# Performance work log

Measured on AMD Instinct MI355X. Metric: run time of the kernel, lower is better.

## Reference

```python
import jax, jax.numpy as jnp
import numpy as np

B, N, D_ATOM, HID, L = 32, 64, 5, 256, 9
E = N * N
F_E = 2 * HID + 2  # [h_i, h_j, d^2, edge_attr]


def _gather(x, idx):
    # x: (B, N, D), idx: (B, E) -> (B, E, D)
    return jax.vmap(lambda a, i: a[i])(x, idx)


def _segsum(data, idx, n):
    # per-batch unsorted segment sum over destination node idx
    return jax.vmap(lambda d, i: jax.ops.segment_sum(d, i, num_segments=n))(data, idx)


def _safe_dist(diff):
    # sqrt of squared norm, safe at 0 (masked self-edges) for grads
    return jnp.sqrt(jnp.maximum(jnp.sum(diff ** 2, axis=-1, keepdims=True), 1e-12))


def _remove_mean(x, mask):
    n = jnp.sum(mask, axis=1, keepdims=True)
    return (x - jnp.sum(x, axis=1, keepdims=True) / n) * mask


def setup_inputs() -> dict:
    key = jax.random.key(0)
    ks = iter(jax.random.split(key, 32))

    def W(shape):
        return jax.random.normal(next(ks), shape, jnp.float32) * 0.02

    x_in = jax.random.normal(next(ks), (B, N, 3), jnp.float32)
    h_in = jax.random.uniform(next(ks), (B, N, D_ATOM), dtype=jnp.float32)
    t = jax.random.uniform(next(ks), (B, N, 1), dtype=jnp.float32)
    ii, jj = jnp.meshgrid(jnp.arange(N), jnp.arange(N), indexing='ij')
    edges = jnp.stack([ii.reshape(-1), jj.reshape(-1)], axis=-1).astype(jnp.int32)  # (E,2) all pairs
    edge_indices = jnp.broadcast_to(edges[None], (B, E, 2))
    node_mask = jnp.ones((B, N, 1), jnp.float32)
    em = (edges[:, 0] != edges[:, 1]).astype(jnp.float32)[:, None]  # mask self-edges
    edge_mask = jnp.broadcast_to(em[None], (B, E, 1))
    params = dict(
        win_w=W((D_ATOM + 1, HID)), win_b=jnp.zeros((HID,), jnp.float32),
        wout_w=W((HID, D_ATOM + 1)), wout_b=jnp.zeros((D_ATOM + 1,), jnp.float32),
        we_w1=W((L, F_E, HID)), we_b1=jnp.zeros((L, HID), jnp.float32),
        we_w2=W((L, HID, HID)), we_b2=jnp.zeros((L, HID), jnp.float32),
        attn_w=W((L, HID, 1)), attn_b=jnp.zeros((L, 1), jnp.float32),
        wh_w1=W((L, 2 * HID, HID)), wh_b1=jnp.zeros((L, HID), jnp.float32),
        wh_w2=W((L, HID, HID)), wh_b2=jnp.zeros((L, HID), jnp.float32),
        wx_w1=W((L, F_E, HID)), wx_b1=jnp.zeros((L, HID), jnp.float32),
        wx_w2=W((L, HID, HID)), wx_b2=jnp.zeros((L, HID), jnp.float32),
        wx_w3=W((L, HID, 1)),
    )
    return dict(x_in=x_in, h_in=h_in, t=t, node_mask=node_mask, edge_mask=edge_mask,
                edge_indices=edge_indices, **params)


def reference(x_in, h_in, t, node_mask, edge_mask, edge_indices,
              win_w, win_b, wout_w, wout_b,
              we_w1, we_b1, we_w2, we_b2, attn_w, attn_b,
              wh_w1, wh_b1, wh_w2, wh_b2,
              wx_w1, wx_b1, wx_w2, wx_b2, wx_w3):
    idx_i = edge_indices[..., 0]
    idx_j = edge_indices[..., 1]
    # fixed edge attribute: initial pairwise distance
    d_in = _safe_dist(_gather(x_in, idx_i) - _gather(x_in, idx_j)) * edge_mask
    h0 = jnp.concatenate([h_in, t], axis=-1) @ win_w + win_b

    def block(carry, p):
        x, h = carry
        ew1, eb1, ew2, eb2, aw, ab, hw1, hb1, hw2, hb2, xw1, xb1, xw2, xb2, xw3 = p
        diff = (_gather(x, idx_i) - _gather(x, idx_j)) * edge_mask  # (B,E,3)
        d = _safe_dist(diff)  # (B,E,1)
        feat = jnp.concatenate([_gather(h, idx_i), _gather(h, idx_j), d ** 2, d_in], axis=-1) * edge_mask
        # edge MLP + attention gate, aggregated to node i
        m = jax.nn.silu(jax.nn.silu(feat @ ew1 + eb1) @ ew2 + eb2)
        em_agg = _segsum(jax.nn.sigmoid(m @ aw + ab) * m, idx_i, N)
        h_new = (h + (jax.nn.silu(jnp.concatenate([h, em_agg], axis=-1) @ hw1 + hb1) @ hw2 + hb2)) * node_mask
        # coordinate update (no bias on last layer)
        s = jax.nn.silu(jax.nn.silu(feat @ xw1 + xb1) @ xw2 + xb2) @ xw3  # (B,E,1)
        x_new = (x + _segsum(diff / (d + 1.0) * s, idx_i, N)) * node_mask
        return (x_new, h_new), None

    stacked = (we_w1, we_b1, we_w2, we_b2, attn_w, attn_b,
               wh_w1, wh_b1, wh_w2, wh_b2, wx_w1, wx_b1, wx_w2, wx_b2, wx_w3)
    (x, h), _ = jax.lax.scan(block, (x_in, h0), stacked)
    x_out = _remove_mean((x - x_in) * node_mask, node_mask)
    h_out = ((h @ wout_w + wout_b) * node_mask)[..., :-1]
    return jnp.concatenate([x_out, h_out], axis=-1)
```

## Files before the change

### kernel.cpp

```cpp
#include <hip/hip_runtime.h>
#include <hip/hip_bf16.h>
#include <math.h>


#define NB   32
#define NN   64
#define EPB  4096
#define HID  256
#define NL   9

typedef __attribute__((ext_vector_type(8))) short bfrag;
typedef __attribute__((ext_vector_type(4))) float f32x4;
typedef __attribute__((ext_vector_type(2))) float f32x2;

__device__ __forceinline__ float fast_rcp(float x) { return __builtin_amdgcn_rcpf(x); }
__device__ __forceinline__ float silu_f(float x) { return x * fast_rcp(1.f + __expf(-x)); }
__device__ __forceinline__ float sigm_f(float x) { return fast_rcp(1.f + __expf(-x)); }
__device__ __forceinline__ ushort bf16rne(float x) {
    unsigned u = __builtin_bit_cast(unsigned, x);
    u = (u + 0x7fffu + ((u >> 16) & 1u)) >> 16;
    return (ushort)u;
}
__device__ __forceinline__ float bf16tof(ushort h) {
    unsigned u = ((unsigned)h) << 16;
    return __builtin_bit_cast(float, u);
}
__device__ __forceinline__ unsigned pk2(f32x2 v) {
    float2 f; f.x = v.x; f.y = v.y;
    __hip_bfloat162 t = __float22bfloat162_rn(f);
    unsigned u;
    __builtin_memcpy(&u, &t, 4);
    return u;
}
__device__ __forceinline__ f32x2 fma2(f32x2 a, f32x2 b, f32x2 c) {
    return __builtin_elementwise_fma(a, b, c);
}
__device__ __forceinline__ f32x4 fma4(f32x4 a, f32x4 b, f32x4 c) {
    return __builtin_elementwise_fma(a, b, c);
}
__device__ __forceinline__ f32x2 silu2(f32x2 v) {
    f32x2 e = { __expf(-v.x), __expf(-v.y) };
    f32x2 d = e + (f32x2){1.f, 1.f};
    f32x2 r = { fast_rcp(d.x), fast_rcp(d.y) };
    return v * r;
}
__device__ __forceinline__ f32x4 silu4(f32x4 v) {
    f32x4 e = { __expf(-v.x), __expf(-v.y), __expf(-v.z), __expf(-v.w) };
    f32x4 d = e + (f32x4){1.f, 1.f, 1.f, 1.f};
    f32x4 r = { fast_rcp(d.x), fast_rcp(d.y), fast_rcp(d.z), fast_rcp(d.w) };
    return v * r;
}

__global__ void edm_k0_pre(const float* __restrict__ x_in, const float* __restrict__ h_in,
                           const float* __restrict__ t_in,
                           const float* __restrict__ win_w, const float* __restrict__ win_b,
                           float* __restrict__ h0, float* __restrict__ din_ws,
                           float* __restrict__ x0)
{
    int blk = blockIdx.x, tid = threadIdx.x;
    if (blk < NB * NN) {
        int node = blk;
        float acc = win_b[tid];
        #pragma unroll
        for (int k = 0; k < 5; ++k) acc += h_in[node * 5 + k] * win_w[k * HID + tid];
        acc += t_in[node] * win_w[5 * HID + tid];
        h0[node * HID + tid] = acc;
    } else if (blk < NB * NN + 512) {
        int e = (blk - NB * NN) * 256 + tid;
        int b = e >> 12, r = e & 4095, i = r >> 6, j = r & 63;
        const float* xb = x_in + b * NN * 3;
        float d0 = xb[i*3+0] - xb[j*3+0];
        float d1 = xb[i*3+1] - xb[j*3+1];
        float d2 = xb[i*3+2] - xb[j*3+2];
        float ss = d0*d0 + d1*d1 + d2*d2;
        float d  = sqrtf(fmaxf(ss, 1e-12f));
        din_ws[e] = (i != j) ? d : 0.f;
    } else {
        int idx = (blk - (NB * NN + 512)) * 256 + tid;
        if (idx < NB * NN * 3) x0[idx] = x_in[idx];
    }
}

__global__ void edm_k5_prep(const float* __restrict__ we_w2, const float* __restrict__ wx_w2,
                            ushort* __restrict__ W2Te, ushort* __restrict__ W2Tx)
{
    __shared__ float t_s[64][65];
    int blk = blockIdx.x;
    int mat = blk / 144, rem = blk % 144, l = rem >> 4, tile = rem & 15;
    int kt = tile >> 2, nt = tile & 3;
    const float* src = (mat ? wx_w2 : we_w2) + l * HID * HID;
    ushort* dst = (mat ? W2Tx : W2Te) + l * HID * HID;
    int col = threadIdx.x & 63, rg = threadIdx.x >> 6;
    #pragma unroll
    for (int it = 0; it < 16; ++it) {
        int row = rg * 16 + it;
        t_s[row][col] = src[(kt * 64 + row) * HID + nt * 64 + col];
    }
    __syncthreads();
    #pragma unroll
    for (int it = 0; it < 16; ++it) {
        int n = rg * 16 + it;
        dst[(nt * 64 + n) * HID + kt * 64 + col] = bf16rne(t_s[col][n]);
    }
}

__global__ void edm_k5b_prep(const float* __restrict__ we_w1, const float* __restrict__ wx_w1,
                             ushort* __restrict__ W1Th, ushort* __restrict__ W1Tl)
{
    __shared__ float t_s[64][65];
    int blk = blockIdx.x;
    int tile = blk & 15, out = (blk >> 4) & 3, l = blk >> 6;
    int kt = tile >> 2, nt = tile & 3;
    const float* src = ((out >= 2) ? wx_w1 : we_w1) + l * 514 * HID + (out & 1) * 256 * HID;
    size_t doff = ((size_t)(l * 4 + out)) * HID * HID;
    ushort* dh = W1Th + doff;
    ushort* dl = W1Tl + doff;
    int col = threadIdx.x & 63, rg = threadIdx.x >> 6;
    #pragma unroll
    for (int it = 0; it < 16; ++it) {
        int row = rg * 16 + it;
        t_s[row][col] = src[(kt * 64 + row) * HID + nt * 64 + col];
    }
    __syncthreads();
    #pragma unroll
    for (int it = 0; it < 16; ++it) {
        int n = rg * 16 + it;
        float v = t_s[col][n];
        ushort h = bf16rne(v);
        float lo = v - bf16tof(h);
        dh[(nt * 64 + n) * HID + kt * 64 + col] = h;
        dl[(nt * 64 + n) * HID + kt * 64 + col] = bf16rne(lo);
    }
}

__global__ void edm_k5c_prep(const float* __restrict__ wh_w1, const float* __restrict__ wh_w2,
                             ushort* __restrict__ W3h, ushort* __restrict__ W3l,
                             ushort* __restrict__ W4h, ushort* __restrict__ W4l)
{
    __shared__ float t_s[64][65];
    int blk = blockIdx.x;
    const float* src; ushort* dh; ushort* dl; int kt, nt, Kdim;
    if (blk < 288) {
        int l = blk >> 5, tile = blk & 31;
        kt = tile >> 2; nt = tile & 3; Kdim = 512;
        src = wh_w1 + (size_t)l * 512 * HID;
        dh = W3h + (size_t)l * HID * 512;
        dl = W3l + (size_t)l * HID * 512;
    } else {
        int b2 = blk - 288;
        int l = b2 >> 4, tile = b2 & 15;
        kt = tile >> 2; nt = tile & 3; Kdim = 256;
        src = wh_w2 + (size_t)l * HID * HID;
        dh = W4h + (size_t)l * HID * HID;
        dl = W4l + (size_t)l * HID * HID;
    }
    int col = threadIdx.x & 63, rg = threadIdx.x >> 6;
    #pragma unroll
    for (int it = 0; it < 16; ++it) {
        int row = rg * 16 + it;
        t_s[row][col] = src[(size_t)(kt * 64 + row) * HID + nt * 64 + col];
    }
    __syncthreads();
    #pragma unroll
    for (int it = 0; it < 16; ++it) {
        int n = rg * 16 + it;
        float v = t_s[col][n];
        ushort h = bf16rne(v);
        float lo = v - bf16tof(h);
        dh[(size_t)(nt * 64 + n) * Kdim + kt * 64 + col] = h;
        dl[(size_t)(nt * 64 + n) * Kdim + kt * 64 + col] = bf16rne(lo);
    }
}

__global__ __launch_bounds__(256)
void edm_k1_mfma(const float* __restrict__ h,
                 const ushort* __restrict__ W1Th, const ushort* __restrict__ W1Tl,
                 const float* __restrict__ we_b1, const float* __restrict__ wx_b1,
                 const float* __restrict__ we_w2, const float* __restrict__ we_b2,
                 const float* __restrict__ attn_w, const float* __restrict__ attn_b,
                 float* __restrict__ HeA, float* __restrict__ HeB,
                 float* __restrict__ HxA, float* __restrict__ HxB,
                 float* __restrict__ self_em, int l)
{
    int tid = threadIdx.x;
    if (blockIdx.x == 512) {
        __shared__ float m1s[HID];
        __shared__ float ms[HID];
        __shared__ float wred[4];
        __shared__ float gsh;
        const float* eb1 = we_b1 + l * HID;
        m1s[tid] = silu_f(eb1[tid]);
        __syncthreads();
        const float* W2 = we_w2 + l * HID * HID;
        float acc = we_b2[l * HID + tid];
        for (int k = 0; k < HID; ++k) acc += m1s[k] * W2[k * HID + tid];
        float mv = silu_f(acc);
        ms[tid] = mv;
        float p = mv * attn_w[l * HID + tid];
        #pragma unroll
        for (int off = 32; off > 0; off >>= 1) p += __shfl_down(p, off, 64);
        if ((tid & 63) == 0) wred[tid >> 6] = p;
        __syncthreads();
        if (tid == 0) gsh = sigm_f(wred[0] + wred[1] + wred[2] + wred[3] + attn_b[l]);
        __syncthreads();
        self_em[tid] = gsh * ms[tid];
        return;
    }

    __shared__ __align__(16) ushort Ah_s[16384];
    __shared__ __align__(16) ushort Al_s[16384];

    const int cq = blockIdx.x & 3;
    const int out = (blockIdx.x >> 2) & 3;
    const int ntile = blockIdx.x >> 4;
    const int base = ntile * 64;

    {
        const int c  = tid & 31;
        const int jg = tid >> 5;
        const int k0 = c * 8;
        #pragma unroll
        for (int it = 0; it < 8; ++it) {
            int m = it * 8 + jg;
            f32x4 h0 = *(const f32x4*)&h[(base + m) * HID + k0];
            f32x4 h1 = *(const f32x4*)&h[(base + m) * HID + k0 + 4];
            uint4 phi, plo;
            {
                ushort ax = bf16rne(h0.x), ay = bf16rne(h0.y);
                phi.x = (unsigned)ax | ((unsigned)ay << 16);
                plo.x = pk2((f32x2){h0.x - bf16tof(ax), h0.y - bf16tof(ay)});
            }
            {
                ushort ax = bf16rne(h0.z), ay = bf16rne(h0.w);
                phi.y = (unsigned)ax | ((unsigned)ay << 16);
                plo.y = pk2((f32x2){h0.z - bf16tof(ax), h0.w - bf16tof(ay)});
            }
            {
                ushort ax = bf16rne(h1.x), ay = bf16rne(h1.y);
                phi.z = (unsigned)ax | ((unsigned)ay << 16);
                plo.z = pk2((f32x2){h1.x - bf16tof(ax), h1.y - bf16tof(ay)});
            }
            {
                ushort ax = bf16rne(h1.z), ay = bf16rne(h1.w);
                phi.w = (unsigned)ax | ((unsigned)ay << 16);
                plo.w = pk2((f32x2){h1.z - bf16tof(ax), h1.w - bf16tof(ay)});
            }
            unsigned off = (unsigned)(m * 256 + ((c ^ (m & 7)) * 8));
            *(uint4*)&Ah_s[off] = phi;
            *(uint4*)&Al_s[off] = plo;
        }
    }
    __syncthreads();

    const int w = tid >> 6, lane = tid & 63, quad = lane >> 4, l16 = lane & 15;
    const int col = cq * 64 + w * 16 + l16;
    const ushort* Bh = W1Th + ((size_t)(l * 4 + out)) * HID * HID + (size_t)col * HID;
    const ushort* Bl = W1Tl + ((size_t)(l * 4 + out)) * HID * HID + (size_t)col * HID;

    f32x4 acc[4];
    #pragma unroll
    for (int mt = 0; mt < 4; ++mt) acc[mt] = (f32x4){0.f, 0.f, 0.f, 0.f};

    #pragma unroll
    for (int kt = 0; kt < 8; ++kt) {
        const int kof = kt * 32 + quad * 8;
        const int ch  = (kt * 4 + quad) ^ (l16 & 7);
        bfrag bh = *(const bfrag*)&Bh[kof];
        bfrag bl = *(const bfrag*)&Bl[kof];
        bfrag ahr[4], alr[4];
        #pragma unroll
        for (int mt = 0; mt < 4; ++mt) {
            ahr[mt] = *(const bfrag*)&Ah_s[(mt * 16 + l16) * 256 + ch * 8];
            alr[mt] = *(const bfrag*)&Al_s[(mt * 16 + l16) * 256 + ch * 8];
        }
        #pragma unroll
        for (int mt = 0; mt < 4; ++mt) {
            acc[mt] = __builtin_amdgcn_mfma_f32_16x16x32_bf16(ahr[mt], bh, acc[mt], 0, 0, 0);
            acc[mt] = __builtin_amdgcn_mfma_f32_16x16x32_bf16(ahr[mt], bl, acc[mt], 0, 0, 0);
            acc[mt] = __builtin_amdgcn_mfma_f32_16x16x32_bf16(alr[mt], bh, acc[mt], 0, 0, 0);
        }
    }

    float bias = 0.f;
    if (out == 0) bias = we_b1[l * HID + col];
    else if (out == 2) bias = wx_b1[l * HID + col];
    float* dst = (out == 0) ? HeA : (out == 1) ? HeB : (out == 2) ? HxA : HxB;
    #pragma unroll
    for (int mt = 0; mt < 4; ++mt)
        #pragma unroll
        for (int r = 0; r < 4; ++r)
            dst[(base + mt * 16 + quad * 4 + r) * HID + col] = acc[mt][r] + bias;
}

__global__ __launch_bounds__(256, 4)
void edm_kb_gemm(const float* __restrict__ x_cur, float* __restrict__ x_next,
                 const float* __restrict__ HeA, const float* __restrict__ HeB,
                 const float* __restrict__ HxA, const float* __restrict__ HxB,
                 const float* __restrict__ din_ws,
                 const float* __restrict__ we_w1, const float* __restrict__ we_b1,
                 const float* __restrict__ wx_w1, const float* __restrict__ wx_b1,
                 const ushort* __restrict__ W2Te, const ushort* __restrict__ W2Tx,
                 const float* __restrict__ we_b2, const float* __restrict__ wx_b2,
                 const float* __restrict__ attn_w, const float* __restrict__ attn_b,
                 const float* __restrict__ wx_w3,
                 float* __restrict__ em_agg, int l)
{
    __shared__ __align__(16) ushort A_s[16384];
    __shared__ float red_s[256];
    __shared__ float sc_s[64];
    __shared__ float x_s[192];
    __shared__ float d2_s[64], din_s[64];

    const int tid = threadIdx.x;
    const int blk = blockIdx.x;
    const int p = blk >> 11, bi = blk & 2047, b = bi >> 6, i = bi & 63;

    if (tid < 192) x_s[tid] = x_cur[b * 192 + tid];
    __syncthreads();
    if (tid < 64) {
        int j = tid;
        float d0 = x_s[i*3+0] - x_s[j*3+0];
        float d1 = x_s[i*3+1] - x_s[j*3+1];
        float d2 = x_s[i*3+2] - x_s[j*3+2];
        float ss = d0*d0 + d1*d1 + d2*d2;
        float d  = sqrtf(fmaxf(ss, 1e-12f));
        d2_s[j]  = d * d;
        din_s[j] = din_ws[b * EPB + i * 64 + j];
    }
    __syncthreads();

    {
        const float* W1  = (p ? wx_w1 : we_w1) + l * 514 * HID;
        const float* HA  = (p ? HxA : HeA);
        const float* HB  = (p ? HxB : HeB);
        const float* b1p = (p ? wx_b1 : we_b1) + l * HID;

        const int c  = tid & 31;
        const int jg = tid >> 5;
        const int k0 = c * 8;

        f32x4 ra0 = *(const f32x4*)&HA[(b * 64 + i) * HID + k0];
        f32x4 ra1 = *(const f32x4*)&HA[(b * 64 + i) * HID + k0 + 4];
        f32x4 wa0 = *(const f32x4*)&W1[512 * HID + k0];
        f32x4 wa1 = *(const f32x4*)&W1[512 * HID + k0 + 4];
        f32x4 wb0 = *(const f32x4*)&W1[513 * HID + k0];
        f32x4 wb1 = *(const f32x4*)&W1[513 * HID + k0 + 4];
        f32x4 b10 = *(const f32x4*)&b1p[k0];
        f32x4 b11 = *(const f32x4*)&b1p[k0 + 4];
        uint4 pki;
        pki.x = pk2(silu2((f32x2){b10.x, b10.y}));
        pki.y = pk2(silu2((f32x2){b10.z, b10.w}));
        pki.z = pk2(silu2((f32x2){b11.x, b11.y}));
        pki.w = pk2(silu2((f32x2){b11.z, b11.w}));

        const float* hbp = HB + b * 64 * HID + k0;
        #pragma unroll
        for (int it = 0; it < 8; ++it) {
            int j = it * 8 + jg;
            f32x4 h0 = *(const f32x4*)&hbp[j * HID];
            f32x4 h1 = *(const f32x4*)&hbp[j * HID + 4];
            f32x2 dd = { d2_s[j], d2_s[j] };
            f32x2 dn = { din_s[j], din_s[j] };
            uint4 pkv;
            f32x2 v;
            v = fma2(dn, (f32x2){wb0.x, wb0.y},
                 fma2(dd, (f32x2){wa0.x, wa0.y},
                      (f32x2){ra0.x + h0.x, ra0.y + h0.y}));
            pkv.x = pk2(silu2(v));
            v = fma2(dn, (f32x2){wb0.z, wb0.w},
                 fma2(dd, (f32x2){wa0.z, wa0.w},
                      (f32x2){ra0.z + h0.z, ra0.w + h0.w}));
            pkv.y = pk2(silu2(v));
            v = fma2(dn, (f32x2){wb1.x, wb1.y},
                 fma2(dd, (f32x2){wa1.x, wa1.y},
                      (f32x2){ra1.x + h1.x, ra1.y + h1.y}));
            pkv.z = pk2(silu2(v));
            v = fma2(dn, (f32x2){wb1.z, wb1.w},
                 fma2(dd, (f32x2){wa1.z, wa1.w},
                      (f32x2){ra1.z + h1.z, ra1.w + h1.w}));
            pkv.w = pk2(silu2(v));
            if (j == i) pkv = pki;
            *(uint4*)&A_s[j * 256 + (unsigned)((c ^ (j & 7)) * 8)] = pkv;
        }
    }
    __syncthreads();

    const int w = tid >> 6, lane = tid & 63, quad = lane >> 4, l16 = lane & 15;
    const ushort* W2T = (p ? W2Tx : W2Te) + l * HID * HID;
    const int cb0 = w * 64 + l16;
    f32x4 acc[4][4];
    #pragma unroll
    for (int mt = 0; mt < 4; ++mt)
        #pragma unroll
        for (int nt = 0; nt < 4; ++nt) acc[mt][nt] = (f32x4){0.f, 0.f, 0.f, 0.f};

    #pragma unroll
    for (int kt = 0; kt < 8; ++kt) {
        const int kof = kt * 32 + quad * 8;
        const int ch  = (kt * 4 + quad) ^ (l16 & 7);
        bfrag bfr[4], afr[4];
        #pragma unroll
        for (int nt = 0; nt < 4; ++nt)
            bfr[nt] = *(const bfrag*)&W2T[(cb0 + nt * 16) * HID + kof];
        #pragma unroll
        for (int mt = 0; mt < 4; ++mt)
            afr[mt] = *(const bfrag*)&A_s[(mt * 16 + l16) * 256 + ch * 8];
        #pragma unroll
        for (int mt = 0; mt < 4; ++mt)
            #pragma unroll
            for (int nt = 0; nt < 4; ++nt)
                acc[mt][nt] = __builtin_amdgcn_mfma_f32_16x16x32_bf16(
                    afr[mt], bfr[nt], acc[mt][nt], 0, 0, 0);
    }

    const float* b2p = (p ? wx_b2 : we_b2) + l * HID;
    const float* vvp = p ? (wx_w3 + l * HID) : (attn_w + l * HID);
    float b2v[4], vv[4];
    #pragma unroll
    for (int nt = 0; nt < 4; ++nt) { b2v[nt] = b2p[cb0 + nt * 16]; vv[nt] = vvp[cb0 + nt * 16]; }

    #pragma unroll
    for (int mt = 0; mt < 4; ++mt)
        #pragma unroll
        for (int nt = 0; nt < 4; ++nt) {
            f32x4 bb = { b2v[nt], b2v[nt], b2v[nt], b2v[nt] };
            acc[mt][nt] = silu4(acc[mt][nt] + bb);
        }

    #pragma unroll
    for (int mt = 0; mt < 4; ++mt) {
        f32x4 t4 = acc[mt][0] * (f32x4){vv[0], vv[0], vv[0], vv[0]};
        t4 = fma4(acc[mt][1], (f32x4){vv[1], vv[1], vv[1], vv[1]}, t4);
        t4 = fma4(acc[mt][2], (f32x4){vv[2], vv[2], vv[2], vv[2]}, t4);
        t4 = fma4(acc[mt][3], (f32x4){vv[3], vv[3], vv[3], vv[3]}, t4);
        #pragma unroll
        for (int r = 0; r < 4; ++r) {
            float pd = t4[r];
            pd += __shfl_xor(pd, 1, 64); pd += __shfl_xor(pd, 2, 64);
            pd += __shfl_xor(pd, 4, 64); pd += __shfl_xor(pd, 8, 64);
            if (l16 == 0) red_s[w * 64 + mt * 16 + quad * 4 + r] = pd;
        }
    }
    __syncthreads();
    if (tid < 64) {
        float tot = red_s[tid] + red_s[64 + tid] + red_s[128 + tid] + red_s[192 + tid];
        if (p == 0) sc_s[tid] = (tid == i) ? 0.f : sigm_f(tot + attn_b[l]);
        else        sc_s[tid] = tot;
    }
    __syncthreads();

    if (p == 0) {
        f32x4 g[4];
        #pragma unroll
        for (int mt = 0; mt < 4; ++mt) g[mt] = *(const f32x4*)&sc_s[mt * 16 + quad * 4];
        #pragma unroll
        for (int nt = 0; nt < 4; ++nt) {
            f32x4 e4 = g[0] * acc[0][nt];
            e4 = fma4(g[1], acc[1][nt], e4);
            e4 = fma4(g[2], acc[2][nt], e4);
            e4 = fma4(g[3], acc[3][nt], e4);
            float e = (e4.x + e4.y) + (e4.z + e4.w);
            e += __shfl_xor(e, 16, 64); e += __shfl_xor(e, 32, 64);
            if (quad == 0) em_agg[(b * 64 + i) * HID + cb0 + nt * 16] = e;
        }
    } else {
        if (tid < 64) {
            int j = tid;
            float d0 = x_s[i*3+0] - x_s[j*3+0];
            float d1 = x_s[i*3+1] - x_s[j*3+1];
            float d2 = x_s[i*3+2] - x_s[j*3+2];
            float ss = d0*d0 + d1*d1 + d2*d2;
            float d  = sqrtf(fmaxf(ss, 1e-12f));
            float f  = fast_rcp(d + 1.f) * sc_s[j];
            float cx = d0 * f, cy = d1 * f, cz = d2 * f;
            #pragma unroll
            for (int off = 32; off > 0; off >>= 1) {
                cx += __shfl_down(cx, off, 64);
                cy += __shfl_down(cy, off, 64);
                cz += __shfl_down(cz, off, 64);
            }
            if (tid == 0) {
                x_next[bi * 3 + 0] = x_s[i*3+0] + cx;
                x_next[bi * 3 + 1] = x_s[i*3+1] + cy;
                x_next[bi * 3 + 2] = x_s[i*3+2] + cz;
            }
        }
    }
}

__global__ __launch_bounds__(256)
void edm_k3_mfma(const float* __restrict__ h, const float* __restrict__ em_agg,
                 const float* __restrict__ self_em,
                 const ushort* __restrict__ W3h, const ushort* __restrict__ W3l,
                 const float* __restrict__ wh_b1,
                 const ushort* __restrict__ W4h, const ushort* __restrict__ W4l,
                 const float* __restrict__ wh_b2,
                 float* __restrict__ h_next, int l)
{
    __shared__ __align__(16) ushort Ah_s[16 * 512];
    __shared__ __align__(16) ushort Al_s[16 * 512];
    __shared__ __align__(16) ushort Uh_s[16 * 256];
    __shared__ __align__(16) ushort Ul_s[16 * 256];

    const int tid = threadIdx.x;
    const int base = blockIdx.x * 16;

    {
        const int c  = tid & 63;
        const int jg = tid >> 6;
        const int k0 = c * 8;
        #pragma unroll
        for (int t = 0; t < 4; ++t) {
            int m = t * 4 + jg;
            f32x4 v0, v1;
            if (c < 32) {
                v0 = *(const f32x4*)&h[(base + m) * HID + k0];
                v1 = *(const f32x4*)&h[(base + m) * HID + k0 + 4];
            } else {
                int e0 = k0 - 256;
                f32x4 a0 = *(const f32x4*)&em_agg[(base + m) * HID + e0];
                f32x4 a1 = *(const f32x4*)&em_agg[(base + m) * HID + e0 + 4];
                f32x4 s0 = *(const f32x4*)&self_em[e0];
                f32x4 s1 = *(const f32x4*)&self_em[e0 + 4];
                v0 = a0 + s0; v1 = a1 + s1;
            }
            uint4 phi, plo;
            {
                ushort ax = bf16rne(v0.x), ay = bf16rne(v0.y);
                phi.x = (unsigned)ax | ((unsigned)ay << 16);
                plo.x = pk2((f32x2){v0.x - bf16tof(ax), v0.y - bf16tof(ay)});
            }
            {
                ushort ax = bf16rne(v0.z), ay = bf16rne(v0.w);
                phi.y = (unsigned)ax | ((unsigned)ay << 16);
                plo.y = pk2((f32x2){v0.z - bf16tof(ax), v0.w - bf16tof(ay)});
            }
            {
                ushort ax = bf16rne(v1.x), ay = bf16rne(v1.y);
                phi.z = (unsigned)ax | ((unsigned)ay << 16);
                plo.z = pk2((f32x2){v1.x - bf16tof(ax), v1.y - bf16tof(ay)});
            }
            {
                ushort ax = bf16rne(v1.z), ay = bf16rne(v1.w);
                phi.w = (unsigned)ax | ((unsigned)ay << 16);
                plo.w = pk2((f32x2){v1.z - bf16tof(ax), v1.w - bf16tof(ay)});
            }
            unsigned off = (unsigned)(m * 512 + ((c ^ (m & 7)) * 8));
            *(uint4*)&Ah_s[off] = phi;
            *(uint4*)&Al_s[off] = plo;
        }
    }
    __syncthreads();

    const int w = tid >> 6, lane = tid & 63, quad = lane >> 4, l16 = lane & 15;

    f32x4 acc1[4];
    #pragma unroll
    for (int nt = 0; nt < 4; ++nt) acc1[nt] = (f32x4){0.f, 0.f, 0.f, 0.f};

    for (int ks = 0; ks < 16; ++ks) {
        const int kof = ks * 32 + quad * 8;
        unsigned aoff = (unsigned)(l16 * 512 + (((ks * 4 + quad) ^ (l16 & 7))) * 8);
        bfrag ah = *(const bfrag*)&Ah_s[aoff];
        bfrag al = *(const bfrag*)&Al_s[aoff];
        #pragma unroll
        for (int nt = 0; nt < 4; ++nt) {
            int col = w * 64 + nt * 16 + l16;
            bfrag bh = *(const bfrag*)&W3h[((size_t)l * HID + col) * 512 + kof];
            bfrag bl = *(const bfrag*)&W3l[((size_t)l * HID + col) * 512 + kof];
            acc1[nt] = __builtin_amdgcn_mfma_f32_16x16x32_bf16(ah, bh, acc1[nt], 0, 0, 0);
            acc1[nt] = __builtin_amdgcn_mfma_f32_16x16x32_bf16(ah, bl, acc1[nt], 0, 0, 0);
            acc1[nt] = __builtin_amdgcn_mfma_f32_16x16x32_bf16(al, bh, acc1[nt], 0, 0, 0);
        }
    }

    #pragma unroll
    for (int nt = 0; nt < 4; ++nt) {
        int colv = w * 64 + nt * 16 + l16;
        float b1v = wh_b1[l * HID + colv];
        #pragma unroll
        for (int r = 0; r < 4; ++r) {
            float u = silu_f(acc1[nt][r] + b1v);
            ushort uh = bf16rne(u);
            float ulo = u - bf16tof(uh);
            int row = quad * 4 + r;
            unsigned ao = (unsigned)(row * 256 + (((colv >> 3) ^ (row & 7))) * 8 + (colv & 7));
            Uh_s[ao] = uh;
            Ul_s[ao] = bf16rne(ulo);
        }
    }
    __syncthreads();

    f32x4 acc2[4];
    #pragma unroll
    for (int nt = 0; nt < 4; ++nt) acc2[nt] = (f32x4){0.f, 0.f, 0.f, 0.f};

    #pragma unroll
    for (int kt = 0; kt < 8; ++kt) {
        const int kof = kt * 32 + quad * 8;
        unsigned aoff = (unsigned)(l16 * 256 + (((kt * 4 + quad) ^ (l16 & 7))) * 8);
        bfrag ah = *(const bfrag*)&Uh_s[aoff];
        bfrag al = *(const bfrag*)&Ul_s[aoff];
        #pragma unroll
        for (int nt = 0; nt < 4; ++nt) {
            int col = w * 64 + nt * 16 + l16;
            bfrag bh = *(const bfrag*)&W4h[((size_t)l * HID + col) * HID + kof];
            bfrag bl = *(const bfrag*)&W4l[((size_t)l * HID + col) * HID + kof];
            acc2[nt] = __builtin_amdgcn_mfma_f32_16x16x32_bf16(ah, bh, acc2[nt], 0, 0, 0);
            acc2[nt] = __builtin_amdgcn_mfma_f32_16x16x32_bf16(ah, bl, acc2[nt], 0, 0, 0);
            acc2[nt] = __builtin_amdgcn_mfma_f32_16x16x32_bf16(al, bh, acc2[nt], 0, 0, 0);
        }
    }

    #pragma unroll
    for (int nt = 0; nt < 4; ++nt) {
        int colv = w * 64 + nt * 16 + l16;
        float b2v = wh_b2[l * HID + colv];
        #pragma unroll
        for (int r = 0; r < 4; ++r) {
            int node = base + quad * 4 + r;
            h_next[node * HID + colv] = h[node * HID + colv] + acc2[nt][r] + b2v;
        }
    }
}

__global__ void edm_k4_out(const float* __restrict__ x_fin, const float* __restrict__ x_in,
                           const float* __restrict__ h_fin,
                           const float* __restrict__ wout_w, const float* __restrict__ wout_b,
                           float* __restrict__ out)
{
    __shared__ float vx[192];
    __shared__ float mean_s[3];
    int b = blockIdx.x, tid = threadIdx.x;
    if (tid < 192) vx[tid] = x_fin[b * 192 + tid] - x_in[b * 192 + tid];
    __syncthreads();
    if (tid < 3) {
        float s = 0.f;
        for (int n = 0; n < 64; ++n) s += vx[n * 3 + tid];
        mean_s[tid] = s * (1.f / 64.f);
    }
    __syncthreads();
    if (tid < 192) out[b * 512 + (tid / 3) * 8 + (tid % 3)] = vx[tid] - mean_s[tid % 3];

    int node = tid / 5, ch = tid % 5;
    float acc = wout_b[ch];
    const float* hr = h_fin + (b * 64 + node) * HID;
    for (int k = 0; k < HID; ++k) acc = fmaf(hr[k], wout_w[k * 6 + ch], acc);
    out[b * 512 + node * 8 + 3 + ch] = acc;
}

extern "C" void kernel_launch(void* const* d_in, const int* in_sizes, int n_in,
                              void* d_out, int out_size, void* d_ws, size_t ws_size,
                              hipStream_t stream)
{
    const float* x_in   = (const float*)d_in[0];
    const float* h_in   = (const float*)d_in[1];
    const float* t_in   = (const float*)d_in[2];
    const float* win_w  = (const float*)d_in[6];
    const float* win_b  = (const float*)d_in[7];
    const float* wout_w = (const float*)d_in[8];
    const float* wout_b = (const float*)d_in[9];
    const float* we_w1  = (const float*)d_in[10];
    const float* we_b1  = (const float*)d_in[11];
    const float* we_w2  = (const float*)d_in[12];
    const float* we_b2  = (const float*)d_in[13];
    const float* attn_w = (const float*)d_in[14];
    const float* attn_b = (const float*)d_in[15];
    const float* wh_w1  = (const float*)d_in[16];
    const float* wh_b1  = (const float*)d_in[17];
    const float* wh_w2  = (const float*)d_in[18];
    const float* wh_b2  = (const float*)d_in[19];
    const float* wx_w1  = (const float*)d_in[20];
    const float* wx_b1  = (const float*)d_in[21];
    const float* wx_w2  = (const float*)d_in[22];
    const float* wx_b2  = (const float*)d_in[23];
    const float* wx_w3  = (const float*)d_in[24];

    float* ws = (float*)d_ws;
    const size_t SN = (size_t)NB * NN * HID;
    float* h_a = ws;
    float* h_b = ws + SN;
    float* HeA = ws + 2 * SN;
    float* HeB = ws + 3 * SN;
    float* HxA = ws + 4 * SN;
    float* HxB = ws + 5 * SN;
    float* emg = ws + 6 * SN;
    float* din = ws + 7 * SN;
    float* x_a = din + (size_t)NB * EPB;
    float* x_b = x_a + NB * NN * 3;
    float* sem = x_b + NB * NN * 3;
    ushort* W2Te = (ushort*)(sem + 256);
    ushort* W2Tx = W2Te + (size_t)NL * HID * HID;
    ushort* W1Th = W2Tx + (size_t)NL * HID * HID;
    ushort* W1Tl = W1Th + (size_t)NL * 4 * HID * HID;
    ushort* W3h  = W1Tl + (size_t)NL * 4 * HID * HID;
    ushort* W3l  = W3h + (size_t)NL * HID * 512;
    ushort* W4h  = W3l + (size_t)NL * HID * 512;
    ushort* W4l  = W4h + (size_t)NL * HID * HID;

    edm_k5_prep<<<dim3(288), dim3(256), 0, stream>>>(we_w2, wx_w2, W2Te, W2Tx);
    edm_k5b_prep<<<dim3(576), dim3(256), 0, stream>>>(we_w1, wx_w1, W1Th, W1Tl);
    edm_k5c_prep<<<dim3(432), dim3(256), 0, stream>>>(wh_w1, wh_w2, W3h, W3l, W4h, W4l);

    edm_k0_pre<<<dim3(NB * NN + 512 + 24), dim3(256), 0, stream>>>(
        x_in, h_in, t_in, win_w, win_b, h_a, din, x_a);

    for (int l = 0; l < NL; ++l) {
        float* h_cur = (l & 1) ? h_b : h_a;
        float* h_nxt = (l & 1) ? h_a : h_b;
        float* x_cur = (l & 1) ? x_b : x_a;
        float* x_nxt = (l & 1) ? x_a : x_b;

        edm_k1_mfma<<<dim3(513), dim3(256), 0, stream>>>(
            h_cur, W1Th, W1Tl, we_b1, wx_b1, we_w2, we_b2, attn_w, attn_b,
            HeA, HeB, HxA, HxB, sem, l);

        edm_kb_gemm<<<dim3(2 * NB * NN), dim3(256), 0, stream>>>(
            x_cur, x_nxt, HeA, HeB, HxA, HxB, din,
            we_w1, we_b1, wx_w1, wx_b1, W2Te, W2Tx,
            we_b2, wx_b2, attn_w, attn_b, wx_w3, emg, l);

        edm_k3_mfma<<<dim3(128), dim3(256), 0, stream>>>(
            h_cur, emg, sem, W3h, W3l, wh_b1, W4h, W4l, wh_b2, h_nxt, l);
    }

    edm_k4_out<<<dim3(NB), dim3(320), 0, stream>>>(
        x_b, x_in, h_b, wout_w, wout_b, (float*)d_out);
}
```

Measured before the change: 1.273 ms.

## Split node-update MLP into two kernels with column-quartered grids for more parallelism

The fused node-update kernel ran only 128 blocks, each computing all 256 output columns of both GEMMs. It is now split into two kernels, each launched with 512 blocks that own a 64-column quarter. The intermediate activation is written to global memory as swizzled hi/lo bf16 buffers instead of LDS. This is meant to fill more compute units on the small GEMM. In exchange it adds a kernel launch per layer, a global round trip for the intermediate, and makes each block repeat the A-tile load and split.

```diff
diff --git a/kernel.cpp b/kernel.cpp
--- a/kernel.cpp
+++ b/kernel.cpp
@@ -489,21 +489,18 @@
 }
 
 __global__ __launch_bounds__(256)
-void edm_k3_mfma(const float* __restrict__ h, const float* __restrict__ em_agg,
-                 const float* __restrict__ self_em,
-                 const ushort* __restrict__ W3h, const ushort* __restrict__ W3l,
-                 const float* __restrict__ wh_b1,
-                 const ushort* __restrict__ W4h, const ushort* __restrict__ W4l,
-                 const float* __restrict__ wh_b2,
-                 float* __restrict__ h_next, int l)
+void edm_k3a(const float* __restrict__ h, const float* __restrict__ em_agg,
+             const float* __restrict__ self_em,
+             const ushort* __restrict__ W3h, const ushort* __restrict__ W3l,
+             const float* __restrict__ wh_b1,
+             ushort* __restrict__ Uh, ushort* __restrict__ Ul, int l)
 {
     __shared__ __align__(16) ushort Ah_s[16 * 512];
     __shared__ __align__(16) ushort Al_s[16 * 512];
-    __shared__ __align__(16) ushort Uh_s[16 * 256];
-    __shared__ __align__(16) ushort Ul_s[16 * 256];
 
     const int tid = threadIdx.x;
-    const int base = blockIdx.x * 16;
+    const int cq = blockIdx.x & 3;
+    const int base = (blockIdx.x >> 2) * 16;
 
     {
         const int c  = tid & 63;
@@ -553,74 +550,74 @@
     __syncthreads();
 
     const int w = tid >> 6, lane = tid & 63, quad = lane >> 4, l16 = lane & 15;
-
-    f32x4 acc1[4];
-    #pragma unroll
-    for (int nt = 0; nt < 4; ++nt) acc1[nt] = (f32x4){0.f, 0.f, 0.f, 0.f};
+    const int colv = cq * 64 + w * 16 + l16;
+
+    f32x4 acc = (f32x4){0.f, 0.f, 0.f, 0.f};
+    const ushort* Bh = W3h + ((size_t)l * HID + colv) * 512;
+    const ushort* Bl = W3l + ((size_t)l * HID + colv) * 512;
 
     for (int ks = 0; ks < 16; ++ks) {
         const int kof = ks * 32 + quad * 8;
         unsigned aoff = (unsigned)(l16 * 512 + (((ks * 4 + quad) ^ (l16 & 7))) * 8);
         bfrag ah = *(const bfrag*)&Ah_s[aoff];
         bfrag al = *(const bfrag*)&Al_s[aoff];
-        #pragma unroll
-        for (int nt = 0; nt < 4; ++nt) {
-            int col = w * 64 + nt * 16 + l16;
-            bfrag bh = *(const bfrag*)&W3h[((size_t)l * HID + col) * 512 + kof];
-            bfrag bl = *(const bfrag*)&W3l[((size_t)l * HID + col) * 512 + kof];
-            acc1[nt] = __builtin_amdgcn_mfma_f32_16x16x32_bf16(ah, bh, acc1[nt], 0, 0, 0);
-            acc1[nt] = __builtin_amdgcn_mfma_f32_16x16x32_bf16(ah, bl, acc1[nt], 0, 0, 0);
-            acc1[nt] = __builtin_amdgcn_mfma_f32_16x16x32_bf16(al, bh, acc1[nt], 0, 0, 0);
-        }
-    }
-
-    #pragma unroll
-    for (int nt = 0; nt < 4; ++nt) {
-        int colv = w * 64 + nt * 16 + l16;
-        float b1v = wh_b1[l * HID + colv];
-        #pragma unroll
-        for (int r = 0; r < 4; ++r) {
-            float u = silu_f(acc1[nt][r] + b1v);
-            ushort uh = bf16rne(u);
-            float ulo = u - bf16tof(uh);
-            int row = quad * 4 + r;
-            unsigned ao = (unsigned)(row * 256 + (((colv >> 3) ^ (row & 7))) * 8 + (colv & 7));
-            Uh_s[ao] = uh;
-            Ul_s[ao] = bf16rne(ulo);
-        }
-    }
-    __syncthreads();
-
-    f32x4 acc2[4];
-    #pragma unroll
-    for (int nt = 0; nt < 4; ++nt) acc2[nt] = (f32x4){0.f, 0.f, 0.f, 0.f};
-
+        bfrag bh = *(const bfrag*)&Bh[kof];
+        bfrag bl = *(const bfrag*)&Bl[kof];
+        acc = __builtin_amdgcn_mfma_f32_16x16x32_bf16(ah, bh, acc, 0, 0, 0);
+        acc = __builtin_amdgcn_mfma_f32_16x16x32_bf16(ah, bl, acc, 0, 0, 0);
+        acc = __builtin_amdgcn_mfma_f32_16x16x32_bf16(al, bh, acc, 0, 0, 0);
+    }
+
+    float b1v = wh_b1[l * HID + colv];
+    #pragma unroll
+    for (int r = 0; r < 4; ++r) {
+        float u = silu_f(acc[r] + b1v);
+        ushort uh = bf16rne(u);
+        float ulo = u - bf16tof(uh);
+        int row = quad * 4 + r;
+        size_t ao = (size_t)(base + row) * 256 + (((colv >> 3) ^ (row & 7))) * 8 + (colv & 7);
+        Uh[ao] = uh;
+        Ul[ao] = bf16rne(ulo);
+    }
+}
+
+__global__ __launch_bounds__(256)
+void edm_k3b(const float* __restrict__ h,
+             const ushort* __restrict__ Uh, const ushort* __restrict__ Ul,
+             const ushort* __restrict__ W4h, const ushort* __restrict__ W4l,
+             const float* __restrict__ wh_b2,
+             float* __restrict__ h_next, int l)
+{
+    const int tid = threadIdx.x;
+    const int cq = blockIdx.x & 3;
+    const int base = (blockIdx.x >> 2) * 16;
+    const int w = tid >> 6, lane = tid & 63, quad = lane >> 4, l16 = lane & 15;
+    const int colv = cq * 64 + w * 16 + l16;
+
+    const ushort* Bh = W4h + ((size_t)l * HID + colv) * HID;
+    const ushort* Bl = W4l + ((size_t)l * HID + colv) * HID;
+    const ushort* Ah = Uh + (size_t)(base + l16) * 256;
+    const ushort* Al = Ul + (size_t)(base + l16) * 256;
+
+    f32x4 acc = (f32x4){0.f, 0.f, 0.f, 0.f};
     #pragma unroll
     for (int kt = 0; kt < 8; ++kt) {
         const int kof = kt * 32 + quad * 8;
-        unsigned aoff = (unsigned)(l16 * 256 + (((kt * 4 + quad) ^ (l16 & 7))) * 8);
-        bfrag ah = *(const bfrag*)&Uh_s[aoff];
-        bfrag al = *(const bfrag*)&Ul_s[aoff];
-        #pragma unroll
-        for (int nt = 0; nt < 4; ++nt) {
-            int col = w * 64 + nt * 16 + l16;
-            bfrag bh = *(const bfrag*)&W4h[((size_t)l * HID + col) * HID + kof];
-            bfrag bl = *(const bfrag*)&W4l[((size_t)l * HID + col) * HID + kof];
-            acc2[nt] = __builtin_amdgcn_mfma_f32_16x16x32_bf16(ah, bh, acc2[nt], 0, 0, 0);
-            acc2[nt] = __builtin_amdgcn_mfma_f32_16x16x32_bf16(ah, bl, acc2[nt], 0, 0, 0);
-            acc2[nt] = __builtin_amdgcn_mfma_f32_16x16x32_bf16(al, bh, acc2[nt], 0, 0, 0);
-        }
-    }
-
-    #pragma unroll
-    for (int nt = 0; nt < 4; ++nt) {
-        int colv = w * 64 + nt * 16 + l16;
-        float b2v = wh_b2[l * HID + colv];
-        #pragma unroll
-        for (int r = 0; r < 4; ++r) {
-            int node = base + quad * 4 + r;
-            h_next[node * HID + colv] = h[node * HID + colv] + acc2[nt][r] + b2v;
-        }
+        unsigned ach = (unsigned)((((kt * 4 + quad) ^ (l16 & 7))) * 8);
+        bfrag ah = *(const bfrag*)&Ah[ach];
+        bfrag al = *(const bfrag*)&Al[ach];
+        bfrag bh = *(const bfrag*)&Bh[kof];
+        bfrag bl = *(const bfrag*)&Bl[kof];
+        acc = __builtin_amdgcn_mfma_f32_16x16x32_bf16(ah, bh, acc, 0, 0, 0);
+        acc = __builtin_amdgcn_mfma_f32_16x16x32_bf16(ah, bl, acc, 0, 0, 0);
+        acc = __builtin_amdgcn_mfma_f32_16x16x32_bf16(al, bh, acc, 0, 0, 0);
+    }
+
+    float b2v = wh_b2[l * HID + colv];
+    #pragma unroll
+    for (int r = 0; r < 4; ++r) {
+        int node = base + quad * 4 + r;
+        h_next[node * HID + colv] = h[node * HID + colv] + acc[r] + b2v;
     }
 }
 
@@ -697,6 +694,8 @@
     ushort* W3l  = W3h + (size_t)NL * HID * 512;
     ushort* W4h  = W3l + (size_t)NL * HID * 512;
     ushort* W4l  = W4h + (size_t)NL * HID * HID;
+    ushort* Uh   = W4l + (size_t)NL * HID * HID;
+    ushort* Ul   = Uh + (size_t)NB * NN * HID;
 
     edm_k5_prep<<<dim3(288), dim3(256), 0, stream>>>(we_w2, wx_w2, W2Te, W2Tx);
     edm_k5b_prep<<<dim3(576), dim3(256), 0, stream>>>(we_w1, wx_w1, W1Th, W1Tl);
@@ -720,8 +719,11 @@
             we_w1, we_b1, wx_w1, wx_b1, W2Te, W2Tx,
             we_b2, wx_b2, attn_w, attn_b, wx_w3, emg, l);
 
-        edm_k3_mfma<<<dim3(128), dim3(256), 0, stream>>>(
-            h_cur, emg, sem, W3h, W3l, wh_b1, W4h, W4l, wh_b2, h_nxt, l);
+        edm_k3a<<<dim3(512), dim3(256), 0, stream>>>(
+            h_cur, emg, sem, W3h, W3l, wh_b1, Uh, Ul, l);
+
+        edm_k3b<<<dim3(512), dim3(256), 0, stream>>>(
+            h_cur, Uh, Ul, W4h, W4l, wh_b2, h_nxt, l);
     }
 
     edm_k4_out<<<dim3(NB), dim3(320), 0, stream>>>(
```

Result: faster. 1.199 ms (-5.8%).
